# Kernel optimization log

Hardware: AMD Instinct MI355X
Metric: run time of the kernel (lower is better)

The kernel has to match this reference:

```python
import jax, jax.numpy as jnp
import numpy as np

N_SRC = 1024     # source frames
N_TGT = 100000   # target pool frames
D = 1024         # WavLM layer-6 feature dim
K = 4            # neighbors


def setup_inputs() -> dict:
    key = jax.random.key(0)
    k1, k2 = jax.random.split(key)
    source_feats = jax.random.normal(k1, (N_SRC, D), dtype=jnp.float32)
    target_feats = jax.random.normal(k2, (N_TGT, D), dtype=jnp.float32)
    return {"source_feats": source_feats, "target_feats": target_feats, "k": K}


def reference(source_feats, target_feats, k):
    # Cosine distance kNN: smallest cosine distance == largest cosine similarity.
    s = source_feats / jnp.linalg.norm(source_feats, axis=-1, keepdims=True)
    t = target_feats / jnp.linalg.norm(target_feats, axis=-1, keepdims=True)
    sim = jnp.einsum('nd,md->nm', s, t)          # [N_SRC, N_TGT]
    _, idx = jax.lax.top_k(sim, k)               # [N_SRC, k] neighbor indices
    # Gather ORIGINAL (un-normalized) target rows and average over neighbors,
    # matching sklearn kneighbors + target_np[indices].mean(axis=0).
    gathered = target_feats[idx]                 # [N_SRC, k, D]
    return gathered.mean(axis=1)                 # [N_SRC, D]
```

## Files before the change

### kernel.cpp

```cpp
#include <hip/hip_runtime.h>
#include <hip/hip_bf16.h>
#include <float.h>

#define N_SRC 1024
#define N_TGT 100000
#define DIM   1024
#define KNN   4

#define BM 128
#define BN 256
#define BK 64
#define NKT (DIM / BK)
#define NMB 782
#define N_TGT2 (NMB * BM)
#define NSC (N_SRC / BN)
#define NBLK (NMB * NSC)
#define NSTRIP NMB
#define NCAND (NSTRIP * KNN)
#define RERANK 32

#define SRC_KT_B 65536ull
#define TGT_KT_B ((unsigned long long)N_TGT2 * 64ull)

typedef __attribute__((ext_vector_type(4))) float f32x4;
typedef __attribute__((ext_vector_type(4))) unsigned int u32x4;
typedef __attribute__((ext_vector_type(2))) long long i64x2;

__device__ __forceinline__ void gload16(const void* gp, void* lp) {
    __builtin_amdgcn_global_load_lds(
        (const __attribute__((address_space(1))) void*)gp,
        (__attribute__((address_space(3))) void*)lp, 16, 0, 0);
}

__device__ __forceinline__ unsigned int pk_fp8x4(float x0, float x1,
                                                 float x2, float x3) {
    int d = __builtin_amdgcn_cvt_pk_fp8_f32(x0, x1, 0, false);
    d     = __builtin_amdgcn_cvt_pk_fp8_f32(x2, x3, d, true);
    return (unsigned int)d;
}

__device__ __forceinline__ void ce_desc(float& v1, int& i1, float& v2, int& i2)
{
    bool sw = (v2 > v1) || (v2 == v1 && i2 < i1);
    float tv = sw ? v2 : v1; float uv = sw ? v1 : v2;
    int   ti = sw ? i2 : i1; int   ui = sw ? i1 : i2;
    v1 = tv; i1 = ti; v2 = uv; i2 = ui;
}

__global__ __launch_bounds__(256) void convert_src_kernel(
    const float* __restrict__ src, unsigned int* __restrict__ srcws)
{
    int gid = blockIdx.x * 256 + threadIdx.x;
    int kt  = gid >> 12;
    int rem = gid & 4095;
    int row = rem >> 2;
    int pos = rem & 3;
    int c   = pos ^ ((row >> 1) & 3);
    const float4* p0 = (const float4*)(src + (size_t)row * DIM + kt * BK + c * 8);
    const float4* p1 = (const float4*)(src + (size_t)row * DIM + kt * BK + 32 + c * 8);
    float4 a0 = p0[0], a1 = p0[1], b0 = p1[0], b1 = p1[1];
    u32x4 o = { pk_fp8x4(a0.x, a0.y, a0.z, a0.w),
                pk_fp8x4(a1.x, a1.y, a1.z, a1.w),
                pk_fp8x4(b0.x, b0.y, b0.z, b0.w),
                pk_fp8x4(b1.x, b1.y, b1.z, b1.w) };
    ((u32x4*)srcws)[gid] = o;
}

__global__ __launch_bounds__(256) void prep_tgt_kernel(
    const float* __restrict__ tgt, unsigned int* __restrict__ tgtbf,
    float* __restrict__ invnw)
{
    __shared__ float pn[16][17];
    const int t  = threadIdx.x;
    const int li = t & 15;
    const int kt = t >> 4;
    const int row = blockIdx.x * 16 + li;
    const bool valid = row < N_TGT;

    float4 v[16];
    if (valid) {
        const float4* p = (const float4*)(tgt + (size_t)row * DIM + kt * BK);
        #pragma unroll
        for (int i = 0; i < 16; ++i) v[i] = p[i];
    } else {
        #pragma unroll
        for (int i = 0; i < 16; ++i) v[i] = make_float4(0.f, 0.f, 0.f, 0.f);
    }
    float nsq = 0.f;
    #pragma unroll
    for (int i = 0; i < 16; ++i)
        nsq += v[i].x * v[i].x + v[i].y * v[i].y
             + v[i].z * v[i].z + v[i].w * v[i].w;

    u32x4* o = (u32x4*)((char*)tgtbf + (size_t)kt * TGT_KT_B
                        + (size_t)row * 64);
    const int f = (row >> 1) & 3;
    #pragma unroll
    for (int c = 0; c < 4; ++c) {
        float4 a0 = v[2 * c], a1 = v[2 * c + 1];
        float4 b0 = v[8 + 2 * c], b1 = v[8 + 2 * c + 1];
        o[c ^ f] = (u32x4){ pk_fp8x4(a0.x, a0.y, a0.z, a0.w),
                            pk_fp8x4(a1.x, a1.y, a1.z, a1.w),
                            pk_fp8x4(b0.x, b0.y, b0.z, b0.w),
                            pk_fp8x4(b1.x, b1.y, b1.z, b1.w) };
    }

    pn[li][kt] = nsq;
    __syncthreads();
    if (t < 16) {
        float s = 0.f;
        #pragma unroll
        for (int k = 0; k < 16; ++k) s += pn[t][k];
        int r2 = blockIdx.x * 16 + t;
        invnw[r2] = (r2 < N_TGT) ? 1.0f / sqrtf(s) : -1.0f;
    }
}

__global__ __launch_bounds__(512, 4) void gemm_topk_fp8_kernel(
    const void* __restrict__ tgtbf, const void* __restrict__ srcbf,
    const float* __restrict__ invnw,
    float* __restrict__ cand_val, int* __restrict__ cand_idx)
{
    __shared__ __align__(16) unsigned char As[2][BM][BK];
    __shared__ __align__(16) unsigned char Bs[2][BN][BK];
    __shared__ float invn_sh[BM];
    __shared__ float scv[2 * BN * KNN];
    __shared__ int   sci[2 * BN * KNN];

    const int b = blockIdx.x;
    const int logical = (b & 7) * (NBLK / 8) + (b >> 3);
    const int mblk = logical >> 2;
    const int schk = logical & 3;
    const int m0 = mblk * BM;
    const int c0 = schk * BN;

    const int t = threadIdx.x;
    const int lane = t & 63;
    const int w = t >> 6;
    const int wm = w >> 2, wn = w & 3;
    const int g = lane >> 4, li = lane & 15;

    const char* tb_ = (const char*)tgtbf;
    const char* sb_ = (const char*)srcbf;

    f32x4 acc[4][4];
    #pragma unroll
    for (int i = 0; i < 4; ++i)
        #pragma unroll
        for (int j = 0; j < 4; ++j) acc[i][j] = (f32x4){0.f, 0.f, 0.f, 0.f};

    unsigned char *Ac = &As[0][0][0], *An = &As[1][0][0];
    unsigned char *Bc = &Bs[0][0][0], *Bn = &Bs[1][0][0];

    #define STAGE(Ab_, Bb_, kt_) do {                                         \
        const char* ga_ = tb_ + (size_t)(kt_) * TGT_KT_B + (size_t)m0 * 64    \
                          + (size_t)t * 16;                                   \
        gload16(ga_, (Ab_) + t * 16);                                         \
        const char* gb_ = sb_ + (size_t)(kt_) * SRC_KT_B + (size_t)c0 * 64    \
                          + (size_t)t * 16;                                   \
        gload16(gb_,        (Bb_) + t * 16);                                  \
        gload16(gb_ + 8192, (Bb_) + 8192 + t * 16);                           \
    } while (0)

    const int sl = (g ^ ((li >> 1) & 3)) * 16;

    #define READ_AB do {                                                      \
        _Pragma("unroll")                                                     \
        for (int mf = 0; mf < 4; ++mf)                                        \
            af[mf] = *(const i64x2*)(Ac + (wm * 64 + mf * 16 + li) * BK + sl);\
        _Pragma("unroll")                                                     \
        for (int nf = 0; nf < 4; ++nf)                                        \
            bf[nf] = *(const i64x2*)(Bc + (wn * 64 + nf * 16 + li) * BK + sl);\
    } while (0)

    #define DO_MFMA do {                                                      \
        _Pragma("unroll")                                                     \
        for (int mf = 0; mf < 4; ++mf)                                        \
            _Pragma("unroll")                                                 \
            for (int nf = 0; nf < 4; ++nf)                                    \
                acc[mf][nf] = __builtin_amdgcn_mfma_f32_16x16x32_fp8_fp8(     \
                    af[mf][0], bf[nf][0], acc[mf][nf], 0, 0, 0);              \
        _Pragma("unroll")                                                     \
        for (int mf = 0; mf < 4; ++mf)                                        \
            _Pragma("unroll")                                                 \
            for (int nf = 0; nf < 4; ++nf)                                    \
                acc[mf][nf] = __builtin_amdgcn_mfma_f32_16x16x32_fp8_fp8(     \
                    af[mf][1], bf[nf][1], acc[mf][nf], 0, 0, 0);              \
    } while (0)

    STAGE(Ac, Bc, 0);
    __syncthreads();

    for (int kt = 0; kt < NKT; ++kt) {
        if (kt + 1 < NKT) STAGE(An, Bn, kt + 1);
        i64x2 af[4], bf[4];
        READ_AB;
        DO_MFMA;
        __syncthreads();
        unsigned char* tmp_;
        tmp_ = Ac; Ac = An; An = tmp_;
        tmp_ = Bc; Bc = Bn; Bn = tmp_;
    }
    #undef STAGE
    #undef READ_AB
    #undef DO_MFMA

    if (t < BM) invn_sh[t] = invnw[m0 + t];
    __syncthreads();

    float invr[4][4];
    #pragma unroll
    for (int mf = 0; mf < 4; ++mf)
        #pragma unroll
        for (int j = 0; j < 4; ++j)
            invr[mf][j] = invn_sh[wm * 64 + mf * 16 + g * 4 + j];

    #pragma unroll
    for (int nf = 0; nf < 4; ++nf) {
        const int col = wn * 64 + nf * 16 + li;
        float s[4][4];
        #pragma unroll
        for (int mf = 0; mf < 4; ++mf)
            #pragma unroll
            for (int j = 0; j < 4; ++j)
                s[mf][j] = (invr[mf][j] > 0.f) ? acc[mf][nf][j] * invr[mf][j]
                                               : -FLT_MAX;
        #pragma unroll
        for (int it = 0; it < KNN; ++it) {
            float bv = -FLT_MAX; int bli = 0;
            #pragma unroll
            for (int mf = 0; mf < 4; ++mf)
                #pragma unroll
                for (int j = 0; j < 4; ++j) {
                    int id = mf * 16 + g * 4 + j;
                    if (s[mf][j] > bv) { bv = s[mf][j]; bli = id; }
                }
            #pragma unroll
            for (int off = 16; off < 64; off <<= 1) {
                float ov = __shfl_xor(bv, off);
                int   oi = __shfl_xor(bli, off);
                if (ov > bv || (ov == bv && oi < bli)) { bv = ov; bli = oi; }
            }
            const int mfw = bli >> 4, gw = (bli >> 2) & 3, jw = bli & 3;
            if (g == gw) {
                #pragma unroll
                for (int mf = 0; mf < 4; ++mf)
                    #pragma unroll
                    for (int j = 0; j < 4; ++j)
                        if (mf == mfw && j == jw) s[mf][j] = -FLT_MAX;
            }
            if (g == it) {
                int o = (wm * BN + col) * KNN + it;
                scv[o] = bv;
                sci[o] = m0 + wm * 64 + bli;
            }
        }
    }
    __syncthreads();

    if (t < BN) {
        float v4[4] = { -FLT_MAX, -FLT_MAX, -FLT_MAX, -FLT_MAX };
        int   i4[4] = { 0x7fffffff, 0x7fffffff, 0x7fffffff, 0x7fffffff };
        #pragma unroll
        for (int q = 0; q < 8; ++q) {
            int o = ((q >> 2) * BN + t) * KNN + (q & 3);
            float v = scv[o]; int ix = sci[o];
            if (v > v4[3] || (v == v4[3] && ix < i4[3])) {
                v4[3] = v; i4[3] = ix;
                ce_desc(v4[2], i4[2], v4[3], i4[3]);
                ce_desc(v4[1], i4[1], v4[2], i4[2]);
                ce_desc(v4[0], i4[0], v4[1], i4[1]);
            }
        }
        size_t o = ((size_t)(c0 + t) * NSTRIP + mblk) * KNN;
        #pragma unroll
        for (int it = 0; it < KNN; ++it) {
            cand_val[o + it] = v4[it];
            cand_idx[o + it] = i4[it];
        }
    }
}

__global__ __launch_bounds__(256) void merge_rerank_kernel(
    const float* __restrict__ src, const float* __restrict__ tgt,
    const float* __restrict__ cand_val, const int* __restrict__ cand_idx,
    float* __restrict__ out)
{
    __shared__ float sv[NCAND];
    __shared__ float red_v[4];
    __shared__ int   red_p[4];
    __shared__ int   topi[RERANK];
    __shared__ float rsim[RERANK];
    __shared__ int   ridx[RERANK];
    __shared__ int   sel[KNN];

    const int row = blockIdx.x;
    const int t = threadIdx.x, lane = t & 63, w = t >> 6;
    const float* cv = cand_val + (size_t)row * NCAND;
    const int*   ci = cand_idx + (size_t)row * NCAND;

    for (int i = t; i < NCAND; i += 256) sv[i] = cv[i];
    __syncthreads();

    for (int it = 0; it < RERANK; ++it) {
        float bv = -FLT_MAX; int bp = 0;
        for (int i = t; i < NCAND; i += 256) {
            float v = sv[i];
            if (v > bv) { bv = v; bp = i; }
        }
        #pragma unroll
        for (int off = 1; off < 64; off <<= 1) {
            float ov = __shfl_xor(bv, off);
            int   op = __shfl_xor(bp, off);
            if (ov > bv || (ov == bv && op < bp)) { bv = ov; bp = op; }
        }
        if (lane == 0) { red_v[w] = bv; red_p[w] = bp; }
        __syncthreads();
        if (t == 0) {
            float Bv = red_v[0]; int Bp = red_p[0];
            for (int q = 1; q < 4; ++q)
                if (red_v[q] > Bv || (red_v[q] == Bv && red_p[q] < Bp)) {
                    Bv = red_v[q]; Bp = red_p[q];
                }
            topi[it] = ci[Bp];
            sv[Bp] = -FLT_MAX;
        }
        __syncthreads();
    }

    const float4* sp = (const float4*)(src + (size_t)row * DIM);
    #pragma unroll
    for (int q = 0; q < 8; ++q) {
        int cidx = topi[w + 4 * q];
        const float4* tp = (const float4*)(tgt + (size_t)cidx * DIM);
        float a = 0.f, nn = 0.f;
        #pragma unroll
        for (int p = 0; p < 4; ++p) {
            float4 x = sp[lane + 64 * p], y = tp[lane + 64 * p];
            a  = fmaf(x.x, y.x, a);  a  = fmaf(x.y, y.y, a);
            a  = fmaf(x.z, y.z, a);  a  = fmaf(x.w, y.w, a);
            nn = fmaf(y.x, y.x, nn); nn = fmaf(y.y, y.y, nn);
            nn = fmaf(y.z, y.z, nn); nn = fmaf(y.w, y.w, nn);
        }
        #pragma unroll
        for (int off = 1; off < 64; off <<= 1) {
            a  += __shfl_xor(a, off);
            nn += __shfl_xor(nn, off);
        }
        if (lane == 0) { rsim[w + 4 * q] = a / sqrtf(nn); ridx[w + 4 * q] = cidx; }
    }
    __syncthreads();

    if (w == 0) {
        float v = (lane < RERANK) ? rsim[lane] : -FLT_MAX;
        int  ix = (lane < RERANK) ? ridx[lane] : 0x7fffffff;
        #pragma unroll
        for (int it = 0; it < KNN; ++it) {
            float bv = v; int bix = ix;
            #pragma unroll
            for (int off = 1; off < 32; off <<= 1) {
                float ov = __shfl_xor(bv, off);
                int   oi = __shfl_xor(bix, off);
                if (ov > bv || (ov == bv && oi < bix)) { bv = ov; bix = oi; }
            }
            if (lane == 0) sel[it] = bix;
            if (ix == bix) v = -FLT_MAX;
        }
    }
    __syncthreads();

    const float4* g0 = (const float4*)(tgt + (size_t)sel[0] * DIM);
    const float4* g1 = (const float4*)(tgt + (size_t)sel[1] * DIM);
    const float4* g2 = (const float4*)(tgt + (size_t)sel[2] * DIM);
    const float4* g3 = (const float4*)(tgt + (size_t)sel[3] * DIM);
    float4* po = (float4*)(out + (size_t)row * DIM);
    float4 v0 = g0[t], v1 = g1[t], v2 = g2[t], v3 = g3[t];
    float4 rr;
    rr.x = (v0.x + v1.x + v2.x + v3.x) * 0.25f;
    rr.y = (v0.y + v1.y + v2.y + v3.y) * 0.25f;
    rr.z = (v0.z + v1.z + v2.z + v3.z) * 0.25f;
    rr.w = (v0.w + v1.w + v2.w + v3.w) * 0.25f;
    po[t] = rr;
}

extern "C" void kernel_launch(void* const* d_in, const int* in_sizes, int n_in,
                              void* d_out, int out_size, void* d_ws, size_t ws_size,
                              hipStream_t stream)
{
    const float* src = (const float*)d_in[0];
    const float* tgt = (const float*)d_in[1];
    float* out = (float*)d_out;

    const size_t SRCBF_B = 2097152;
    const size_t TGTBF_B = (size_t)N_TGT2 * 1024;
    const size_t INVN_B  = (size_t)N_TGT2 * 4;
    const size_t CV_B    = (size_t)N_SRC * NCAND * 4;

    char* p = (char*)d_ws;
    unsigned int* srcbf = (unsigned int*)p;
    unsigned int* tgtbf = (unsigned int*)(p + SRCBF_B);
    float* invnw    = (float*)(p + SRCBF_B + TGTBF_B);
    float* cand_val = (float*)(p + SRCBF_B + TGTBF_B + INVN_B);
    int*   cand_idx = (int*)(p + SRCBF_B + TGTBF_B + INVN_B + CV_B);

    convert_src_kernel<<<256, 256, 0, stream>>>(src, srcbf);
    prep_tgt_kernel<<<N_TGT2 / 16, 256, 0, stream>>>(tgt, tgtbf, invnw);
    gemm_topk_fp8_kernel<<<NBLK, 512, 0, stream>>>(tgtbf, srcbf, invnw,
                                                   cand_val, cand_idx);
    merge_rerank_kernel<<<N_SRC, 256, 0, stream>>>(src, tgt,
                                                   cand_val, cand_idx, out);
}
```

Measured before the change: 388.4 us.

## Triple-buffer LDS staging with partial vmcnt waits and alias top-k scratch

Moves the fp8 GEMM main loop from double to triple buffering. Each iteration issues the load for tile kt+2 and waits with s_waitcnt vmcnt(3), so only the older stage must land before the barrier. This keeps more global-to-LDS traffic in flight behind the MFMA work. The extra staging buffers raise LDS use, so the top-k scratch arrays now alias the A buffers after the loop. This relies on the hand-written vmcnt counts matching the three loads per stage.

```diff
diff --git a/kernel.cpp b/kernel.cpp
--- a/kernel.cpp
+++ b/kernel.cpp
@@ -121,11 +121,9 @@
     const float* __restrict__ invnw,
     float* __restrict__ cand_val, int* __restrict__ cand_idx)
 {
-    __shared__ __align__(16) unsigned char As[2][BM][BK];
-    __shared__ __align__(16) unsigned char Bs[2][BN][BK];
+    __shared__ __align__(16) unsigned char As[3][BM][BK];
+    __shared__ __align__(16) unsigned char Bs[3][BN][BK];
     __shared__ float invn_sh[BM];
-    __shared__ float scv[2 * BN * KNN];
-    __shared__ int   sci[2 * BN * KNN];
 
     const int b = blockIdx.x;
     const int logical = (b & 7) * (NBLK / 8) + (b >> 3);
@@ -149,8 +147,8 @@
         #pragma unroll
         for (int j = 0; j < 4; ++j) acc[i][j] = (f32x4){0.f, 0.f, 0.f, 0.f};
 
-    unsigned char *Ac = &As[0][0][0], *An = &As[1][0][0];
-    unsigned char *Bc = &Bs[0][0][0], *Bn = &Bs[1][0][0];
+    unsigned char *Ac = &As[0][0][0], *An1 = &As[1][0][0], *An2 = &As[2][0][0];
+    unsigned char *Bc = &Bs[0][0][0], *Bn1 = &Bs[1][0][0], *Bn2 = &Bs[2][0][0];
 
     #define STAGE(Ab_, Bb_, kt_) do {                                         \
         const char* ga_ = tb_ + (size_t)(kt_) * TGT_KT_B + (size_t)m0 * 64    \
@@ -188,22 +186,50 @@
                     af[mf][1], bf[nf][1], acc[mf][nf], 0, 0, 0);              \
     } while (0)
 
+    #define ROTATE do {                                                       \
+        unsigned char* tmp_;                                                  \
+        tmp_ = Ac; Ac = An1; An1 = An2; An2 = tmp_;                           \
+        tmp_ = Bc; Bc = Bn1; Bn1 = Bn2; Bn2 = tmp_;                           \
+    } while (0)
+
     STAGE(Ac, Bc, 0);
-    __syncthreads();
-
-    for (int kt = 0; kt < NKT; ++kt) {
-        if (kt + 1 < NKT) STAGE(An, Bn, kt + 1);
+    STAGE(An1, Bn1, 1);
+    asm volatile("s_waitcnt vmcnt(3)" ::: "memory");
+    __builtin_amdgcn_sched_barrier(0);
+    __builtin_amdgcn_s_barrier();
+
+    for (int kt = 0; kt < NKT - 2; ++kt) {
+        STAGE(An2, Bn2, kt + 2);
+        i64x2 af[4], bf[4];
+        READ_AB;
+        DO_MFMA;
+        asm volatile("s_waitcnt vmcnt(3)" ::: "memory");
+        __builtin_amdgcn_sched_barrier(0);
+        __builtin_amdgcn_s_barrier();
+        ROTATE;
+    }
+    {
+        i64x2 af[4], bf[4];
+        READ_AB;
+        DO_MFMA;
+        asm volatile("s_waitcnt vmcnt(0)" ::: "memory");
+        __builtin_amdgcn_sched_barrier(0);
+        __builtin_amdgcn_s_barrier();
+        ROTATE;
+    }
+    {
         i64x2 af[4], bf[4];
         READ_AB;
         DO_MFMA;
         __syncthreads();
-        unsigned char* tmp_;
-        tmp_ = Ac; Ac = An; An = tmp_;
-        tmp_ = Bc; Bc = Bn; Bn = tmp_;
     }
     #undef STAGE
     #undef READ_AB
     #undef DO_MFMA
+    #undef ROTATE
+
+    float* scv = (float*)&As[0][0][0];
+    int*   sci = (int*)&As[1][0][0];
 
     if (t < BM) invn_sh[t] = invnw[m0 + t];
     __syncthreads();
```

Result: no change. 387.9 us (-0.1%).

## Switch FP8 GEMM to 32x32x64 scaled MFMA with matching fragment layout

Applied to the files above, without the earlier changes.

Replaces the 16x16x32 fp8 MFMA tiles with the gfx950 scaled 32x32x64 f8f6f4 MFMA using unit scales. This means fewer, larger matrix instructions and wider LDS fragment reads. The conversion kernels now pack 16 contiguous floats per lane to match the new K ordering. The top-k epilogue is rewritten for the 32x32 accumulator layout, so it needs only one cross-half shuffle. The candidate scratch buffers now alias the A tile's LDS, which lowers LDS usage but adds risk in the layout and index mapping.

```diff
diff --git a/kernel.cpp b/kernel.cpp
--- a/kernel.cpp
+++ b/kernel.cpp
@@ -22,9 +22,13 @@
 #define SRC_KT_B 65536ull
 #define TGT_KT_B ((unsigned long long)N_TGT2 * 64ull)
 
-typedef __attribute__((ext_vector_type(4))) float f32x4;
-typedef __attribute__((ext_vector_type(4))) unsigned int u32x4;
-typedef __attribute__((ext_vector_type(2))) long long i64x2;
+#define SCALE1 0x7f7f7f7f
+
+typedef __attribute__((ext_vector_type(4)))  float f32x4;
+typedef __attribute__((ext_vector_type(16))) float f32x16;
+typedef __attribute__((ext_vector_type(4)))  unsigned int u32x4;
+typedef __attribute__((ext_vector_type(4)))  int i32x4;
+typedef __attribute__((ext_vector_type(8)))  int i32x8;
 
 __device__ __forceinline__ void gload16(const void* gp, void* lp) {
     __builtin_amdgcn_global_load_lds(
@@ -32,10 +36,9 @@
         (__attribute__((address_space(3))) void*)lp, 16, 0, 0);
 }
 
-__device__ __forceinline__ unsigned int pk_fp8x4(float x0, float x1,
-                                                 float x2, float x3) {
-    int d = __builtin_amdgcn_cvt_pk_fp8_f32(x0, x1, 0, false);
-    d     = __builtin_amdgcn_cvt_pk_fp8_f32(x2, x3, d, true);
+__device__ __forceinline__ unsigned int pk_fp8x4(float4 v) {
+    int d = __builtin_amdgcn_cvt_pk_fp8_f32(v.x, v.y, 0, false);
+    d     = __builtin_amdgcn_cvt_pk_fp8_f32(v.z, v.w, d, true);
     return (unsigned int)d;
 }
 
@@ -56,13 +59,8 @@
     int row = rem >> 2;
     int pos = rem & 3;
     int c   = pos ^ ((row >> 1) & 3);
-    const float4* p0 = (const float4*)(src + (size_t)row * DIM + kt * BK + c * 8);
-    const float4* p1 = (const float4*)(src + (size_t)row * DIM + kt * BK + 32 + c * 8);
-    float4 a0 = p0[0], a1 = p0[1], b0 = p1[0], b1 = p1[1];
-    u32x4 o = { pk_fp8x4(a0.x, a0.y, a0.z, a0.w),
-                pk_fp8x4(a1.x, a1.y, a1.z, a1.w),
-                pk_fp8x4(b0.x, b0.y, b0.z, b0.w),
-                pk_fp8x4(b1.x, b1.y, b1.z, b1.w) };
+    const float4* p = (const float4*)(src + (size_t)row * DIM + kt * BK + c * 16);
+    u32x4 o = { pk_fp8x4(p[0]), pk_fp8x4(p[1]), pk_fp8x4(p[2]), pk_fp8x4(p[3]) };
     ((u32x4*)srcws)[gid] = o;
 }
 
@@ -97,12 +95,8 @@
     const int f = (row >> 1) & 3;
     #pragma unroll
     for (int c = 0; c < 4; ++c) {
-        float4 a0 = v[2 * c], a1 = v[2 * c + 1];
-        float4 b0 = v[8 + 2 * c], b1 = v[8 + 2 * c + 1];
-        o[c ^ f] = (u32x4){ pk_fp8x4(a0.x, a0.y, a0.z, a0.w),
-                            pk_fp8x4(a1.x, a1.y, a1.z, a1.w),
-                            pk_fp8x4(b0.x, b0.y, b0.z, b0.w),
-                            pk_fp8x4(b1.x, b1.y, b1.z, b1.w) };
+        o[c ^ f] = (u32x4){ pk_fp8x4(v[4 * c + 0]), pk_fp8x4(v[4 * c + 1]),
+                            pk_fp8x4(v[4 * c + 2]), pk_fp8x4(v[4 * c + 3]) };
     }
 
     pn[li][kt] = nsq;
@@ -124,8 +118,6 @@
     __shared__ __align__(16) unsigned char As[2][BM][BK];
     __shared__ __align__(16) unsigned char Bs[2][BN][BK];
     __shared__ float invn_sh[BM];
-    __shared__ float scv[2 * BN * KNN];
-    __shared__ int   sci[2 * BN * KNN];
 
     const int b = blockIdx.x;
     const int logical = (b & 7) * (NBLK / 8) + (b >> 3);
@@ -138,16 +130,19 @@
     const int lane = t & 63;
     const int w = t >> 6;
     const int wm = w >> 2, wn = w & 3;
-    const int g = lane >> 4, li = lane & 15;
+    const int l31 = lane & 31;
+    const int h = lane >> 5;
 
     const char* tb_ = (const char*)tgtbf;
     const char* sb_ = (const char*)srcbf;
 
-    f32x4 acc[4][4];
-    #pragma unroll
-    for (int i = 0; i < 4; ++i)
-        #pragma unroll
-        for (int j = 0; j < 4; ++j) acc[i][j] = (f32x4){0.f, 0.f, 0.f, 0.f};
+    f32x16 acc[2][2];
+    #pragma unroll
+    for (int i = 0; i < 2; ++i)
+        #pragma unroll
+        for (int j = 0; j < 2; ++j)
+            #pragma unroll
+            for (int r = 0; r < 16; ++r) acc[i][j][r] = 0.f;
 
     unsigned char *Ac = &As[0][0][0], *An = &As[1][0][0];
     unsigned char *Bc = &Bs[0][0][0], *Bn = &Bs[1][0][0];
@@ -162,30 +157,32 @@
         gload16(gb_ + 8192, (Bb_) + 8192 + t * 16);                           \
     } while (0)
 
-    const int sl = (g ^ ((li >> 1) & 3)) * 16;
+    const int sw8 = (l31 >> 1) & 3;
+    const int pA = ((2 * h + 0) ^ sw8) * 16;
+    const int pB = ((2 * h + 1) ^ sw8) * 16;
+
+    #define READ_FRAG(dst_, base_, rowoff_) do {                              \
+        i32x4 lo_ = *(const i32x4*)((base_) + (rowoff_) + pA);                \
+        i32x4 hi_ = *(const i32x4*)((base_) + (rowoff_) + pB);                \
+        dst_[0] = lo_[0]; dst_[1] = lo_[1]; dst_[2] = lo_[2]; dst_[3] = lo_[3];\
+        dst_[4] = hi_[0]; dst_[5] = hi_[1]; dst_[6] = hi_[2]; dst_[7] = hi_[3];\
+    } while (0)
 
     #define READ_AB do {                                                      \
-        _Pragma("unroll")                                                     \
-        for (int mf = 0; mf < 4; ++mf)                                        \
-            af[mf] = *(const i64x2*)(Ac + (wm * 64 + mf * 16 + li) * BK + sl);\
-        _Pragma("unroll")                                                     \
-        for (int nf = 0; nf < 4; ++nf)                                        \
-            bf[nf] = *(const i64x2*)(Bc + (wn * 64 + nf * 16 + li) * BK + sl);\
+        READ_FRAG(afr[0], Ac, (wm * 64 +  0 + l31) * BK);                     \
+        READ_FRAG(afr[1], Ac, (wm * 64 + 32 + l31) * BK);                     \
+        READ_FRAG(bfr[0], Bc, (wn * 64 +  0 + l31) * BK);                     \
+        READ_FRAG(bfr[1], Bc, (wn * 64 + 32 + l31) * BK);                     \
     } while (0)
 
     #define DO_MFMA do {                                                      \
         _Pragma("unroll")                                                     \
-        for (int mf = 0; mf < 4; ++mf)                                        \
+        for (int mi = 0; mi < 2; ++mi)                                        \
             _Pragma("unroll")                                                 \
-            for (int nf = 0; nf < 4; ++nf)                                    \
-                acc[mf][nf] = __builtin_amdgcn_mfma_f32_16x16x32_fp8_fp8(     \
-                    af[mf][0], bf[nf][0], acc[mf][nf], 0, 0, 0);              \
-        _Pragma("unroll")                                                     \
-        for (int mf = 0; mf < 4; ++mf)                                        \
-            _Pragma("unroll")                                                 \
-            for (int nf = 0; nf < 4; ++nf)                                    \
-                acc[mf][nf] = __builtin_amdgcn_mfma_f32_16x16x32_fp8_fp8(     \
-                    af[mf][1], bf[nf][1], acc[mf][nf], 0, 0, 0);              \
+            for (int ni = 0; ni < 2; ++ni)                                    \
+                acc[mi][ni] = __builtin_amdgcn_mfma_scale_f32_32x32x64_f8f6f4(\
+                    afr[mi], bfr[ni], acc[mi][ni],                            \
+                    0, 0, 0, SCALE1, 0, SCALE1);                              \
     } while (0)
 
     STAGE(Ac, Bc, 0);
@@ -193,7 +190,7 @@
 
     for (int kt = 0; kt < NKT; ++kt) {
         if (kt + 1 < NKT) STAGE(An, Bn, kt + 1);
-        i64x2 af[4], bf[4];
+        i32x8 afr[2], bfr[2];
         READ_AB;
         DO_MFMA;
         __syncthreads();
@@ -202,57 +199,63 @@
         tmp_ = Bc; Bc = Bn; Bn = tmp_;
     }
     #undef STAGE
+    #undef READ_FRAG
     #undef READ_AB
     #undef DO_MFMA
 
+    float* scv = (float*)&As[0][0][0];
+    int*   sci = (int*)&As[1][0][0];
+
     if (t < BM) invn_sh[t] = invnw[m0 + t];
     __syncthreads();
 
-    float invr[4][4];
-    #pragma unroll
-    for (int mf = 0; mf < 4; ++mf)
-        #pragma unroll
-        for (int j = 0; j < 4; ++j)
-            invr[mf][j] = invn_sh[wm * 64 + mf * 16 + g * 4 + j];
-
-    #pragma unroll
-    for (int nf = 0; nf < 4; ++nf) {
-        const int col = wn * 64 + nf * 16 + li;
-        float s[4][4];
-        #pragma unroll
-        for (int mf = 0; mf < 4; ++mf)
+    float invr[2][16];
+    #pragma unroll
+    for (int mi = 0; mi < 2; ++mi)
+        #pragma unroll
+        for (int r = 0; r < 16; ++r)
+            invr[mi][r] = invn_sh[wm * 64 + mi * 32 + (r & 3) + 8 * (r >> 2)
+                                  + 4 * h];
+
+    #pragma unroll
+    for (int ni = 0; ni < 2; ++ni) {
+        const int col = wn * 64 + ni * 32 + l31;
+        float s[2][16];
+        #pragma unroll
+        for (int mi = 0; mi < 2; ++mi)
             #pragma unroll
-            for (int j = 0; j < 4; ++j)
-                s[mf][j] = (invr[mf][j] > 0.f) ? acc[mf][nf][j] * invr[mf][j]
+            for (int r = 0; r < 16; ++r)
+                s[mi][r] = (invr[mi][r] > 0.f) ? acc[mi][ni][r] * invr[mi][r]
                                                : -FLT_MAX;
         #pragma unroll
         for (int it = 0; it < KNN; ++it) {
-            float bv = -FLT_MAX; int bli = 0;
+            float bv = -FLT_MAX; int bid = 0;
             #pragma unroll
-            for (int mf = 0; mf < 4; ++mf)
+            for (int mi = 0; mi < 2; ++mi)
                 #pragma unroll
-                for (int j = 0; j < 4; ++j) {
-                    int id = mf * 16 + g * 4 + j;
-                    if (s[mf][j] > bv) { bv = s[mf][j]; bli = id; }
+                for (int r = 0; r < 16; ++r) {
+                    int id = mi * 32 + (r & 3) + 8 * (r >> 2) + 4 * h;
+                    if (s[mi][r] > bv) { bv = s[mi][r]; bid = id; }
                 }
-            #pragma unroll
-            for (int off = 16; off < 64; off <<= 1) {
-                float ov = __shfl_xor(bv, off);
-                int   oi = __shfl_xor(bli, off);
-                if (ov > bv || (ov == bv && oi < bli)) { bv = ov; bli = oi; }
+            {
+                float ov = __shfl_xor(bv, 32);
+                int   oi = __shfl_xor(bid, 32);
+                if (ov > bv || (ov == bv && oi < bid)) { bv = ov; bid = oi; }
             }
-            const int mfw = bli >> 4, gw = (bli >> 2) & 3, jw = bli & 3;
-            if (g == gw) {
+            const int hw  = (bid >> 2) & 1;
+            const int miw = bid >> 5;
+            const int rw  = (bid & 3) | (((bid >> 3) & 3) << 2);
+            if (h == hw) {
                 #pragma unroll
-                for (int mf = 0; mf < 4; ++mf)
+                for (int mi = 0; mi < 2; ++mi)
                     #pragma unroll
-                    for (int j = 0; j < 4; ++j)
-                        if (mf == mfw && j == jw) s[mf][j] = -FLT_MAX;
+                    for (int r = 0; r < 16; ++r)
+                        if (mi == miw && r == rw) s[mi][r] = -FLT_MAX;
             }
-            if (g == it) {
+            if (h == 0) {
                 int o = (wm * BN + col) * KNN + it;
                 scv[o] = bv;
-                sci[o] = m0 + wm * 64 + bli;
+                sci[o] = m0 + wm * 64 + bid;
             }
         }
     }
```

New measurement: 1.320 ms. 240% more time.
